# Performance work log

Measured on AMD Instinct MI355X. Metric: run time of the kernel, lower is better.

## Reference

```python
import jax, jax.numpy as jnp
import numpy as np

ALPHA = 2.0  # ATan surrogate alpha (spikingjelly default)
V_TH = 1.0   # v_threshold
H = 8        # num_heads

@jax.custom_vjp
def atan_spike(x):
    # heaviside(v - v_th); x = v - v_th
    return (x >= 0.0).astype(x.dtype)

def _spike_fwd(x):
    return atan_spike(x), x

def _spike_bwd(x, g):
    pi_half = jnp.asarray(np.pi / 2, x.dtype)
    grad = (ALPHA / 2.0) / (1.0 + (pi_half * ALPHA * x) ** 2)
    return (g * grad,)

atan_spike.defvjp(_spike_fwd, _spike_bwd)

def lif(x_seq, w):
    # MultiStepParametricLIFNode: recurrence over leading dim of x_seq.
    # v <- v + (x - (v - v_reset)) * sigmoid(w); v_reset = 0; hard reset, detach_reset=True.
    sg = jax.nn.sigmoid(w)
    def step(v, x):
        h = v + (x - v) * sg
        s = atan_spike(h - V_TH)
        v_new = h * (1.0 - jax.lax.stop_gradient(s))  # hard reset to 0, detached spike
        return v_new, s
    v0 = jnp.zeros_like(x_seq[0])
    _, spikes = jax.lax.scan(step, v0, x_seq)
    return spikes


def setup_inputs() -> dict:
    key = jax.random.key(0)
    ks = jax.random.split(key, 6)
    T, B, N, C = 4, 32, 196, 512
    s = 0.02
    return {
        "x": jax.random.normal(ks[0], (T, B, N, C), dtype=jnp.float32),
        "Wq": jax.random.normal(ks[1], (C, C), dtype=jnp.float32) * s,
        "Wk": jax.random.normal(ks[2], (C, C), dtype=jnp.float32) * s,
        "Wv": jax.random.normal(ks[3], (C, C), dtype=jnp.float32) * s,
        "Wp": jax.random.normal(ks[4], (C, C), dtype=jnp.float32) * s,
        "bp": jax.random.normal(ks[5], (C,), dtype=jnp.float32) * s,
        "wq": jnp.zeros((), jnp.float32),  # init_tau=2 -> w=0
        "wk": jnp.zeros((), jnp.float32),
        "wv": jnp.zeros((), jnp.float32),
        "wa": jnp.zeros((), jnp.float32),
        "wp": jnp.zeros((), jnp.float32),
    }


def reference(x, Wq, Wk, Wv, Wp, bp, wq, wk, wv, wa, wp):
    T, B, N, C = x.shape
    d = C // H
    scale = d ** (-0.5)
    xf = x.reshape(T * B, N, C)  # LIF steps over T*B (faithful to original flatten(0,1))

    def qkv(W, w_lif):
        y = lif(xf @ W.T, w_lif)                       # [T*B, N, C] binary spikes
        return y.reshape(T, B, N, H, d).transpose(0, 1, 3, 2, 4)  # [T,B,H,N,d]

    q = qkv(Wq, wq)
    k = qkv(Wk, wk)
    v = qkv(Wv, wv)

    attn = jnp.einsum('tbhnd,tbhmd->tbhnm', q, k) * scale   # softmax-free
    y = jnp.einsum('tbhnm,tbhmd->tbhnd', attn, v)           # [T,B,H,N,d]
    y = y.swapaxes(3, 4).reshape(T, B, N, C)                # faithful transpose(3,4).reshape

    y = lif(y, wa)                                          # attn_lif steps over T
    out = lif(y.reshape(T * B, N, C) @ Wp.T + bp, wp)       # proj_lif steps over T*B
    return out.reshape(T, B, N, C)
```

## Files before the change

### kernel.cpp

```cpp
#include <hip/hip_runtime.h>

#define NC 100352
typedef unsigned long long ull;

template <int NMAT, bool BIAS>
__global__ __launch_bounds__(256) void gemm_nt(
    const float* __restrict__ A,
    const float* __restrict__ W0, const float* __restrict__ W1,
    const float* __restrict__ W2, const float* __restrict__ bias,
    float* __restrict__ C0, float* __restrict__ C1, float* __restrict__ C2)
{
    __shared__ float As[16][132];
    __shared__ float Bs[16][132];

    const int chunk = (NMAT * 784) >> 3;
    const int w = ((int)blockIdx.x & 7) * chunk + ((int)blockIdx.x >> 3);
    const int rp = w / (4 * NMAT);
    const int rem = w - rp * (4 * NMAT);
    const int br = rem >> 2;
    const int cb = rem & 3;

    const float* Wb = (NMAT == 1 || br == 0) ? W0 : (br == 1 ? W1 : W2);
    float* Cb = (NMAT == 1 || br == 0) ? C0 : (br == 1 ? C1 : C2);

    const int tid = threadIdx.x;
    const int r0 = tid >> 2;
    const int kq = (tid & 3) << 2;
    const int rg = (tid >> 4) << 2;
    const int cg = (tid & 15) << 2;

    float acc[8][8] = {};
    const float* A0 = A + (size_t)(rp * 128 + r0) * 512 + kq;
    const float* A1 = A0 + (size_t)64 * 512;
    const float* B0 = Wb + (size_t)(cb * 128 + r0) * 512 + kq;
    const float* B1 = B0 + (size_t)64 * 512;

    for (int k0 = 0; k0 < 512; k0 += 16) {
        const float4 a0 = *(const float4*)(A0 + k0);
        const float4 a1 = *(const float4*)(A1 + k0);
        const float4 b0 = *(const float4*)(B0 + k0);
        const float4 b1 = *(const float4*)(B1 + k0);
        __syncthreads();
        As[kq + 0][r0] = a0.x; As[kq + 1][r0] = a0.y; As[kq + 2][r0] = a0.z; As[kq + 3][r0] = a0.w;
        As[kq + 0][r0 + 64] = a1.x; As[kq + 1][r0 + 64] = a1.y; As[kq + 2][r0 + 64] = a1.z; As[kq + 3][r0 + 64] = a1.w;
        Bs[kq + 0][r0] = b0.x; Bs[kq + 1][r0] = b0.y; Bs[kq + 2][r0] = b0.z; Bs[kq + 3][r0] = b0.w;
        Bs[kq + 0][r0 + 64] = b1.x; Bs[kq + 1][r0 + 64] = b1.y; Bs[kq + 2][r0 + 64] = b1.z; Bs[kq + 3][r0 + 64] = b1.w;
        __syncthreads();
#pragma unroll
        for (int k = 0; k < 16; ++k) {
            float av[8], bv[8];
            *(float4*)&av[0] = *(const float4*)&As[k][rg];
            *(float4*)&av[4] = *(const float4*)&As[k][rg + 64];
            *(float4*)&bv[0] = *(const float4*)&Bs[k][cg];
            *(float4*)&bv[4] = *(const float4*)&Bs[k][cg + 64];
#pragma unroll
            for (int i = 0; i < 8; ++i)
#pragma unroll
                for (int j = 0; j < 8; ++j)
                    acc[i][j] = fmaf(av[i], bv[j], acc[i][j]);
        }
    }

#pragma unroll
    for (int ih = 0; ih < 2; ++ih)
#pragma unroll
        for (int i = 0; i < 4; ++i) {
            const int row = rp * 128 + rg + i + ih * 64;
#pragma unroll
            for (int jh = 0; jh < 2; ++jh) {
                const int col = cb * 128 + cg + jh * 64;
                float4 o;
                o.x = acc[ih * 4 + i][jh * 4 + 0];
                o.y = acc[ih * 4 + i][jh * 4 + 1];
                o.z = acc[ih * 4 + i][jh * 4 + 2];
                o.w = acc[ih * 4 + i][jh * 4 + 3];
                if (BIAS) {
                    o.x += bias[col + 0]; o.y += bias[col + 1];
                    o.z += bias[col + 2]; o.w += bias[col + 3];
                }
                *(float4*)&Cb[(size_t)row * 512 + col] = o;
            }
        }
}

__global__ __launch_bounds__(256) void gemm_mask(
    const uint* __restrict__ Am,
    const float* __restrict__ W, const float* __restrict__ bias,
    float* __restrict__ C)
{
    __shared__ float Bs[16][132];

    const int w = ((int)blockIdx.x & 7) * 98 + ((int)blockIdx.x >> 3);
    const int rp = w >> 2;
    const int cb = w & 3;

    const int tid = threadIdx.x;
    const int r0 = tid >> 2;
    const int kq = (tid & 3) << 2;
    const int rg = (tid >> 4) << 2;
    const int cg = (tid & 15) << 2;

    const float* B0 = W + (size_t)(cb * 128 + r0) * 512 + kq;
    const float* B1 = B0 + (size_t)64 * 512;

    const uint* mp[8];
#pragma unroll
    for (int ih = 0; ih < 2; ++ih)
#pragma unroll
        for (int i = 0; i < 4; ++i) {
            const int row = rp * 128 + rg + i + ih * 64;
            const int tb = row / 196;
            const int n = row - tb * 196;
            mp[ih * 4 + i] = Am + (size_t)tb * 3136 + n * 16;
        }

    float acc[8][8] = {};

    for (int k0 = 0; k0 < 512; k0 += 16) {
        const float4 b0 = *(const float4*)(B0 + k0);
        const float4 b1 = *(const float4*)(B1 + k0);
        uint wv[8];
        const int wi = k0 >> 5;
        const int sh = k0 & 16;
#pragma unroll
        for (int m = 0; m < 8; ++m) wv[m] = mp[m][wi] >> sh;
        __syncthreads();
        Bs[kq + 0][r0] = b0.x; Bs[kq + 1][r0] = b0.y;
        Bs[kq + 2][r0] = b0.z; Bs[kq + 3][r0] = b0.w;
        Bs[kq + 0][r0 + 64] = b1.x; Bs[kq + 1][r0 + 64] = b1.y;
        Bs[kq + 2][r0 + 64] = b1.z; Bs[kq + 3][r0 + 64] = b1.w;
        __syncthreads();
#pragma unroll
        for (int k = 0; k < 16; ++k) {
            float bv[8], av[8];
            *(float4*)&bv[0] = *(const float4*)&Bs[k][cg];
            *(float4*)&bv[4] = *(const float4*)&Bs[k][cg + 64];
#pragma unroll
            for (int m = 0; m < 8; ++m)
                av[m] = ((wv[m] >> k) & 1u) ? 1.0f : 0.0f;
#pragma unroll
            for (int i = 0; i < 8; ++i)
#pragma unroll
                for (int j = 0; j < 8; ++j)
                    acc[i][j] = fmaf(av[i], bv[j], acc[i][j]);
        }
    }

#pragma unroll
    for (int ih = 0; ih < 2; ++ih)
#pragma unroll
        for (int i = 0; i < 4; ++i) {
            const int row = rp * 128 + rg + i + ih * 64;
#pragma unroll
            for (int jh = 0; jh < 2; ++jh) {
                const int col = cb * 128 + cg + jh * 64;
                float4 o;
                o.x = acc[ih * 4 + i][jh * 4 + 0] + bias[col + 0];
                o.y = acc[ih * 4 + i][jh * 4 + 1] + bias[col + 1];
                o.z = acc[ih * 4 + i][jh * 4 + 2] + bias[col + 2];
                o.w = acc[ih * 4 + i][jh * 4 + 3] + bias[col + 3];
                *(float4*)&C[(size_t)row * 512 + col] = o;
            }
        }
}

__global__ __launch_bounds__(256) void lif_mask3(
    const float* __restrict__ U0, const float* __restrict__ U1,
    const float* __restrict__ U2,
    const float* __restrict__ wq, const float* __restrict__ wk,
    const float* __restrict__ wv, ull* __restrict__ M)
{
    const int br = blockIdx.x / 392;
    const int blk = blockIdx.x - br * 392;
    const int i = blk * 256 + threadIdx.x;
    const float* U = (br == 0) ? U0 : (br == 1 ? U1 : U2);
    const float wv_ = (br == 0) ? wq[0] : (br == 1 ? wk[0] : wv[0]);
    const float sg = 1.0f / (1.0f + expf(-wv_));
    ull* Mw = M + (size_t)br * 200704 + ((i >> 6) & 7) * 196 + (i >> 9);
    float v = 0.0f;
    for (int t = 0; t < 128; ++t) {
        const float x = U[(size_t)t * NC + i];
        const float h = __fadd_rn(v, __fmul_rn(__fsub_rn(x, v), sg));
        const bool sp = (h >= 1.0f);
        const ull m = __ballot(sp);
        if ((threadIdx.x & 63) == 0) Mw[(size_t)t * 1568] = m;
        v = sp ? 0.0f : h;
    }
}

__global__ __launch_bounds__(256) void lif_out(const float* __restrict__ U,
                                               const float* __restrict__ wp,
                                               float* __restrict__ out)
{
    const int i = blockIdx.x * 256 + threadIdx.x;
    const float sg = 1.0f / (1.0f + expf(-wp[0]));
    float v = 0.0f;
    for (int t = 0; t < 128; ++t) {
        const float x = U[(size_t)t * NC + i];
        const float h = __fadd_rn(v, __fmul_rn(__fsub_rn(x, v), sg));
        const bool sp = (h >= 1.0f);
        out[(size_t)t * NC + i] = sp ? 1.0f : 0.0f;
        v = sp ? 0.0f : h;
    }
}

__global__ __launch_bounds__(256) void attn_fused(const ull* __restrict__ Qm,
                                                  const ull* __restrict__ Km,
                                                  const ull* __restrict__ Vm,
                                                  const float* __restrict__ wa,
                                                  uint* __restrict__ Ym)
{
    const int b = blockIdx.x >> 3;
    const int h = blockIdx.x & 7;
    const int tid = threadIdx.x;
    const int w = tid >> 6;
    const int lane = tid & 63;

    __shared__ ull qrow[256], krow[256], vrow[256];
    __shared__ ull kcol[64][5], vcol[64][5];
    __shared__ ushort G[64][64];
    __shared__ float vstate[196][64];
    __shared__ ull sbm[208];

    const float sg = 1.0f / (1.0f + expf(-wa[0]));

    for (int t = 0; t < 4; ++t) {
        const int tb = t * 32 + b;
        const size_t mb = (size_t)tb * 1568 + (size_t)h * 196;
        if (tid < 196) {
            qrow[tid] = Qm[mb + tid];
            krow[tid] = Km[mb + tid];
            vrow[tid] = Vm[mb + tid];
        } else {
            qrow[tid] = 0; krow[tid] = 0; vrow[tid] = 0;
        }
        __syncthreads();

        {
            ull kc = 0, vc = 0;
#pragma unroll 8
            for (int m = 0; m < 64; ++m) {
                kc |= ((krow[w * 64 + m] >> lane) & 1ull) << m;
                vc |= ((vrow[w * 64 + m] >> lane) & 1ull) << m;
            }
            kcol[lane][w] = kc; vcol[lane][w] = vc;
        }
        __syncthreads();

        for (int p = tid; p < 4096; p += 256) {
            const int d1 = p >> 6, d2 = p & 63;
            const int g = __popcll(kcol[d1][0] & vcol[d2][0]) +
                          __popcll(kcol[d1][1] & vcol[d2][1]) +
                          __popcll(kcol[d1][2] & vcol[d2][2]) +
                          __popcll(kcol[d1][3] & vcol[d2][3]);
            G[d1][d2] = (ushort)g;
        }
        __syncthreads();

        {
            int r = 49 * w;
            const int rend = r + 49;
            for (; r + 1 < rend; r += 2) {
                const ull q0 = qrow[r], q1 = qrow[r + 1];
                const uint a0 = (uint)q0, a1 = (uint)(q0 >> 32);
                const uint b0 = (uint)q1, b1 = (uint)(q1 >> 32);
                uint s0 = 0, s1 = 0;
#pragma unroll
                for (int d = 0; d < 32; ++d) {
                    const uint g = G[d][lane];
                    s0 += ((a0 >> d) & 1u) * g;
                    s1 += ((b0 >> d) & 1u) * g;
                }
#pragma unroll
                for (int d = 0; d < 32; ++d) {
                    const uint g = G[32 + d][lane];
                    s0 += ((a1 >> d) & 1u) * g;
                    s1 += ((b1 >> d) & 1u) * g;
                }
                const float y0 = (float)s0 * 0.125f;
                const float v0 = t ? vstate[r][lane] : 0.0f;
                const float h0 = __fadd_rn(v0, __fmul_rn(__fsub_rn(y0, v0), sg));
                const bool sp0 = h0 >= 1.0f;
                vstate[r][lane] = sp0 ? 0.0f : h0;
                const ull m0 = __ballot(sp0);
                const float y1 = (float)s1 * 0.125f;
                const float v1 = t ? vstate[r + 1][lane] : 0.0f;
                const float h1 = __fadd_rn(v1, __fmul_rn(__fsub_rn(y1, v1), sg));
                const bool sp1 = h1 >= 1.0f;
                vstate[r + 1][lane] = sp1 ? 0.0f : h1;
                const ull m1 = __ballot(sp1);
                if (lane == 0) { sbm[r] = m0; sbm[r + 1] = m1; }
            }
            {
                const ull q0 = qrow[r];
                const uint a0 = (uint)q0, a1 = (uint)(q0 >> 32);
                uint s0 = 0;
#pragma unroll
                for (int d = 0; d < 32; ++d) s0 += ((a0 >> d) & 1u) * (uint)G[d][lane];
#pragma unroll
                for (int d = 0; d < 32; ++d) s0 += ((a1 >> d) & 1u) * (uint)G[32 + d][lane];
                const float y0 = (float)s0 * 0.125f;
                const float v0 = t ? vstate[r][lane] : 0.0f;
                const float h0 = __fadd_rn(v0, __fmul_rn(__fsub_rn(y0, v0), sg));
                const bool sp0 = h0 >= 1.0f;
                vstate[r][lane] = sp0 ? 0.0f : h0;
                const ull m0 = __ballot(sp0);
                if (lane == 0) sbm[r] = m0;
            }
        }
        __syncthreads();

        {
            uint* Yw = Ym + (size_t)tb * 3136 + h * 392;
            for (int wd = tid; wd < 392; wd += 256) {
                const int fb = wd * 32;
                const int e0 = fb / 196;
                const int r0 = fb - e0 * 196;
                const int run = (196 - r0 >= 32) ? 32 : (196 - r0);
                uint word = 0;
                for (int j = 0; j < run; ++j)
                    word |= (uint)((sbm[r0 + j] >> e0) & 1ull) << j;
                for (int j = run; j < 32; ++j)
                    word |= (uint)((sbm[j - run] >> (e0 + 1)) & 1ull) << j;
                Yw[wd] = word;
            }
        }
        __syncthreads();
    }
}

extern "C" void kernel_launch(void* const* d_in, const int* in_sizes, int n_in,
                              void* d_out, int out_size, void* d_ws, size_t ws_size,
                              hipStream_t stream) {
    const float* x  = (const float*)d_in[0];
    const float* Wq = (const float*)d_in[1];
    const float* Wk = (const float*)d_in[2];
    const float* Wv = (const float*)d_in[3];
    const float* Wp = (const float*)d_in[4];
    const float* bp = (const float*)d_in[5];
    const float* wq = (const float*)d_in[6];
    const float* wk = (const float*)d_in[7];
    const float* wv = (const float*)d_in[8];
    const float* wa = (const float*)d_in[9];
    const float* wp = (const float*)d_in[10];
    float* out = (float*)d_out;

    char* ws = (char*)d_ws;
    float* u0 = (float*)ws;
    float* u1 = (float*)(ws + (size_t)51380224);
    float* u2 = (float*)(ws + (size_t)2 * 51380224);
    ull* Qm   = (ull*)(ws + (size_t)3 * 51380224);
    ull* Km   = Qm + 200704;
    ull* Vm   = Km + 200704;
    uint* Ym  = (uint*)(ws + (size_t)3 * 51380224 + (size_t)3 * 1605632);
    float* up = u0;

    gemm_nt<3, false><<<2352, 256, 0, stream>>>(x, Wq, Wk, Wv, nullptr,
                                                u0, u1, u2);
    lif_mask3<<<1176, 256, 0, stream>>>(u0, u1, u2, wq, wk, wv, Qm);

    attn_fused<<<256, 256, 0, stream>>>(Qm, Km, Vm, wa, Ym);

    gemm_mask<<<784, 256, 0, stream>>>(Ym, Wp, bp, up);

    lif_out<<<392, 256, 0, stream>>>(up, wp, out);
}
```

Measured before the change: 878.4 us.

## Double attention threads, halve gemm_mask row tile, batch LIF loads

Result: faster. 820.2 us (-6.6%).

```diff
diff --git a/kernel.cpp b/kernel.cpp
--- a/kernel.cpp
+++ b/kernel.cpp
@@ -90,7 +90,7 @@
 {
     __shared__ float Bs[16][132];
 
-    const int w = ((int)blockIdx.x & 7) * 98 + ((int)blockIdx.x >> 3);
+    const int w = ((int)blockIdx.x & 7) * 196 + ((int)blockIdx.x >> 3);
     const int rp = w >> 2;
     const int cb = w & 3;
 
@@ -103,27 +103,25 @@
     const float* B0 = W + (size_t)(cb * 128 + r0) * 512 + kq;
     const float* B1 = B0 + (size_t)64 * 512;
 
-    const uint* mp[8];
-#pragma unroll
-    for (int ih = 0; ih < 2; ++ih)
-#pragma unroll
-        for (int i = 0; i < 4; ++i) {
-            const int row = rp * 128 + rg + i + ih * 64;
-            const int tb = row / 196;
-            const int n = row - tb * 196;
-            mp[ih * 4 + i] = Am + (size_t)tb * 3136 + n * 16;
-        }
-
-    float acc[8][8] = {};
+    const uint* mp[4];
+#pragma unroll
+    for (int i = 0; i < 4; ++i) {
+        const int row = rp * 64 + rg + i;
+        const int tb = row / 196;
+        const int n = row - tb * 196;
+        mp[i] = Am + (size_t)tb * 3136 + n * 16;
+    }
+
+    float acc[4][8] = {};
 
     for (int k0 = 0; k0 < 512; k0 += 16) {
         const float4 b0 = *(const float4*)(B0 + k0);
         const float4 b1 = *(const float4*)(B1 + k0);
-        uint wv[8];
+        uint wv[4];
         const int wi = k0 >> 5;
         const int sh = k0 & 16;
 #pragma unroll
-        for (int m = 0; m < 8; ++m) wv[m] = mp[m][wi] >> sh;
+        for (int m = 0; m < 4; ++m) wv[m] = mp[m][wi] >> sh;
         __syncthreads();
         Bs[kq + 0][r0] = b0.x; Bs[kq + 1][r0] = b0.y;
         Bs[kq + 2][r0] = b0.z; Bs[kq + 3][r0] = b0.w;
@@ -132,14 +130,14 @@
         __syncthreads();
 #pragma unroll
         for (int k = 0; k < 16; ++k) {
-            float bv[8], av[8];
+            float bv[8], av[4];
             *(float4*)&bv[0] = *(const float4*)&Bs[k][cg];
             *(float4*)&bv[4] = *(const float4*)&Bs[k][cg + 64];
 #pragma unroll
-            for (int m = 0; m < 8; ++m)
+            for (int m = 0; m < 4; ++m)
                 av[m] = ((wv[m] >> k) & 1u) ? 1.0f : 0.0f;
 #pragma unroll
-            for (int i = 0; i < 8; ++i)
+            for (int i = 0; i < 4; ++i)
 #pragma unroll
                 for (int j = 0; j < 8; ++j)
                     acc[i][j] = fmaf(av[i], bv[j], acc[i][j]);
@@ -147,21 +145,19 @@
     }
 
 #pragma unroll
-    for (int ih = 0; ih < 2; ++ih)
-#pragma unroll
-        for (int i = 0; i < 4; ++i) {
-            const int row = rp * 128 + rg + i + ih * 64;
-#pragma unroll
-            for (int jh = 0; jh < 2; ++jh) {
-                const int col = cb * 128 + cg + jh * 64;
-                float4 o;
-                o.x = acc[ih * 4 + i][jh * 4 + 0] + bias[col + 0];
-                o.y = acc[ih * 4 + i][jh * 4 + 1] + bias[col + 1];
-                o.z = acc[ih * 4 + i][jh * 4 + 2] + bias[col + 2];
-                o.w = acc[ih * 4 + i][jh * 4 + 3] + bias[col + 3];
-                *(float4*)&C[(size_t)row * 512 + col] = o;
-            }
-        }
+    for (int i = 0; i < 4; ++i) {
+        const int row = rp * 64 + rg + i;
+#pragma unroll
+        for (int jh = 0; jh < 2; ++jh) {
+            const int col = cb * 128 + cg + jh * 64;
+            float4 o;
+            o.x = acc[i][jh * 4 + 0] + bias[col + 0];
+            o.y = acc[i][jh * 4 + 1] + bias[col + 1];
+            o.z = acc[i][jh * 4 + 2] + bias[col + 2];
+            o.w = acc[i][jh * 4 + 3] + bias[col + 3];
+            *(float4*)&C[(size_t)row * 512 + col] = o;
+        }
+    }
 }
 
 __global__ __launch_bounds__(256) void lif_mask3(
@@ -176,15 +172,21 @@
     const float* U = (br == 0) ? U0 : (br == 1 ? U1 : U2);
     const float wv_ = (br == 0) ? wq[0] : (br == 1 ? wk[0] : wv[0]);
     const float sg = 1.0f / (1.0f + expf(-wv_));
+    const bool l0 = (threadIdx.x & 63) == 0;
     ull* Mw = M + (size_t)br * 200704 + ((i >> 6) & 7) * 196 + (i >> 9);
     float v = 0.0f;
-    for (int t = 0; t < 128; ++t) {
-        const float x = U[(size_t)t * NC + i];
-        const float h = __fadd_rn(v, __fmul_rn(__fsub_rn(x, v), sg));
-        const bool sp = (h >= 1.0f);
-        const ull m = __ballot(sp);
-        if ((threadIdx.x & 63) == 0) Mw[(size_t)t * 1568] = m;
-        v = sp ? 0.0f : h;
+    for (int t0 = 0; t0 < 128; t0 += 4) {
+        float x[4];
+#pragma unroll
+        for (int j = 0; j < 4; ++j) x[j] = U[(size_t)(t0 + j) * NC + i];
+#pragma unroll
+        for (int j = 0; j < 4; ++j) {
+            const float h = __fadd_rn(v, __fmul_rn(__fsub_rn(x[j], v), sg));
+            const bool sp = (h >= 1.0f);
+            const ull m = __ballot(sp);
+            if (l0) Mw[(size_t)(t0 + j) * 1568] = m;
+            v = sp ? 0.0f : h;
+        }
     }
 }
 
@@ -195,16 +197,21 @@
     const int i = blockIdx.x * 256 + threadIdx.x;
     const float sg = 1.0f / (1.0f + expf(-wp[0]));
     float v = 0.0f;
-    for (int t = 0; t < 128; ++t) {
-        const float x = U[(size_t)t * NC + i];
-        const float h = __fadd_rn(v, __fmul_rn(__fsub_rn(x, v), sg));
-        const bool sp = (h >= 1.0f);
-        out[(size_t)t * NC + i] = sp ? 1.0f : 0.0f;
-        v = sp ? 0.0f : h;
-    }
-}
-
-__global__ __launch_bounds__(256) void attn_fused(const ull* __restrict__ Qm,
+    for (int t0 = 0; t0 < 128; t0 += 4) {
+        float x[4];
+#pragma unroll
+        for (int j = 0; j < 4; ++j) x[j] = U[(size_t)(t0 + j) * NC + i];
+#pragma unroll
+        for (int j = 0; j < 4; ++j) {
+            const float h = __fadd_rn(v, __fmul_rn(__fsub_rn(x[j], v), sg));
+            const bool sp = (h >= 1.0f);
+            out[(size_t)(t0 + j) * NC + i] = sp ? 1.0f : 0.0f;
+            v = sp ? 0.0f : h;
+        }
+    }
+}
+
+__global__ __launch_bounds__(512) void attn_fused(const ull* __restrict__ Qm,
                                                   const ull* __restrict__ Km,
                                                   const ull* __restrict__ Vm,
                                                   const float* __restrict__ wa,
@@ -217,7 +224,7 @@
     const int lane = tid & 63;
 
     __shared__ ull qrow[256], krow[256], vrow[256];
-    __shared__ ull kcol[64][5], vcol[64][5];
+    __shared__ uint kcol32[64][4][2], vcol32[64][4][2];
     __shared__ ushort G[64][64];
     __shared__ float vstate[196][64];
     __shared__ ull sbm[208];
@@ -231,35 +238,39 @@
             qrow[tid] = Qm[mb + tid];
             krow[tid] = Km[mb + tid];
             vrow[tid] = Vm[mb + tid];
-        } else {
+        } else if (tid < 256) {
             qrow[tid] = 0; krow[tid] = 0; vrow[tid] = 0;
         }
         __syncthreads();
 
         {
-            ull kc = 0, vc = 0;
+            const int j = w >> 1, half = w & 1;
+            const int base = j * 64 + half * 32;
+            uint kc = 0, vc = 0;
 #pragma unroll 8
-            for (int m = 0; m < 64; ++m) {
-                kc |= ((krow[w * 64 + m] >> lane) & 1ull) << m;
-                vc |= ((vrow[w * 64 + m] >> lane) & 1ull) << m;
-            }
-            kcol[lane][w] = kc; vcol[lane][w] = vc;
-        }
-        __syncthreads();
-
-        for (int p = tid; p < 4096; p += 256) {
+            for (int m = 0; m < 32; ++m) {
+                kc |= (uint)((krow[base + m] >> lane) & 1ull) << m;
+                vc |= (uint)((vrow[base + m] >> lane) & 1ull) << m;
+            }
+            kcol32[lane][j][half] = kc; vcol32[lane][j][half] = vc;
+        }
+        __syncthreads();
+
+        for (int p = tid; p < 4096; p += 512) {
             const int d1 = p >> 6, d2 = p & 63;
-            const int g = __popcll(kcol[d1][0] & vcol[d2][0]) +
-                          __popcll(kcol[d1][1] & vcol[d2][1]) +
-                          __popcll(kcol[d1][2] & vcol[d2][2]) +
-                          __popcll(kcol[d1][3] & vcol[d2][3]);
+            int g = 0;
+#pragma unroll
+            for (int j = 0; j < 4; ++j)
+                g += __popc(kcol32[d1][j][0] & vcol32[d2][j][0]) +
+                     __popc(kcol32[d1][j][1] & vcol32[d2][j][1]);
             G[d1][d2] = (ushort)g;
         }
         __syncthreads();
 
         {
-            int r = 49 * w;
-            const int rend = r + 49;
+            const int rbeg = (w * 196) >> 3;
+            const int rend = ((w + 1) * 196) >> 3;
+            int r = rbeg;
             for (; r + 1 < rend; r += 2) {
                 const ull q0 = qrow[r], q1 = qrow[r + 1];
                 const uint a0 = (uint)q0, a1 = (uint)(q0 >> 32);
@@ -291,7 +302,7 @@
                 const ull m1 = __ballot(sp1);
                 if (lane == 0) { sbm[r] = m0; sbm[r + 1] = m1; }
             }
-            {
+            if (r < rend) {
                 const ull q0 = qrow[r];
                 const uint a0 = (uint)q0, a1 = (uint)(q0 >> 32);
                 uint s0 = 0;
@@ -312,7 +323,7 @@
 
         {
             uint* Yw = Ym + (size_t)tb * 3136 + h * 392;
-            for (int wd = tid; wd < 392; wd += 256) {
+            for (int wd = tid; wd < 392; wd += 512) {
                 const int fb = wd * 32;
                 const int e0 = fb / 196;
                 const int r0 = fb - e0 * 196;
@@ -359,9 +370,9 @@
                                                 u0, u1, u2);
     lif_mask3<<<1176, 256, 0, stream>>>(u0, u1, u2, wq, wk, wv, Qm);
 
-    attn_fused<<<256, 256, 0, stream>>>(Qm, Km, Vm, wa, Ym);
-
-    gemm_mask<<<784, 256, 0, stream>>>(Ym, Wp, bp, up);
+    attn_fused<<<256, 512, 0, stream>>>(Qm, Km, Vm, wa, Ym);
+
+    gemm_mask<<<1568, 256, 0, stream>>>(Ym, Wp, bp, up);
 
     lif_out<<<392, 256, 0, stream>>>(up, wp, out);
 }
```
